# Kernel tuning notes

Measured on AMD Instinct MI355X. Metric: run time of the kernel, lower is better.

The kernel has to match this reference:

```python
import jax, jax.numpy as jnp
import numpy as np

D_MODEL = 1024
NUM_HEADS = 16
HEAD_DIM = D_MODEL // NUM_HEADS


def setup_inputs() -> dict:
    key = jax.random.key(0)
    ks = jax.random.split(key, 11)
    B, S, D = 2, 2048, D_MODEL
    scale = 1.0 / np.sqrt(D)
    inp = {
        "q": jax.random.normal(ks[0], (B, S, D), dtype=jnp.float32),
        "k": jax.random.normal(ks[1], (B, S, D), dtype=jnp.float32),
        "v": jax.random.normal(ks[2], (B, S, D), dtype=jnp.float32),
        # torch nn.Linear weights are [out, in]; y = x @ W.T + b
        "Wq": jax.random.normal(ks[3], (D, D), dtype=jnp.float32) * scale,
        "bq": jnp.zeros((D,), dtype=jnp.float32),
        "Wk": jax.random.normal(ks[4], (D, D), dtype=jnp.float32) * scale,
        "bk": jnp.zeros((D,), dtype=jnp.float32),
        "Wv": jax.random.normal(ks[5], (D, D), dtype=jnp.float32) * scale,
        "bv": jnp.zeros((D,), dtype=jnp.float32),
        "Wo": jax.random.normal(ks[6], (D, D), dtype=jnp.float32) * scale,
        "bo": jnp.zeros((D,), dtype=jnp.float32),
    }
    return inp


def _split_heads(x):
    B, S, D = x.shape
    return x.reshape(B, S, NUM_HEADS, HEAD_DIM).transpose(0, 2, 1, 3)  # [B,H,S,hd]


def reference(q, k, v, Wq, bq, Wk, bk, Wv, bv, Wo, bo):
    B, S, D = q.shape
    qh = _split_heads(q @ Wq.T + bq)
    kh = _split_heads(k @ Wk.T + bk)
    vh = _split_heads(v @ Wv.T + bv)
    # scores: [B,H,S,S], causal mask, softmax
    scores = jnp.einsum("bhqd,bhkd->bhqk", qh, kh) / jnp.sqrt(
        jnp.asarray(HEAD_DIM, dtype=qh.dtype))
    causal = jnp.tril(jnp.ones((S, S), dtype=bool))
    scores = jnp.where(causal[None, None], scores, -jnp.inf)
    attn = jax.nn.softmax(scores, axis=-1)
    out = jnp.einsum("bhqk,bhkd->bhqd", attn, vh)  # [B,H,S,hd]
    out = out.transpose(0, 2, 1, 3).reshape(B, S, D)
    return out @ Wo.T + bo
```

## Files before the change

kernel.cpp:

```cpp
#include <hip/hip_runtime.h>
#include <hip/hip_bf16.h>
#include <cstdint>
#include <cstddef>

typedef __bf16 bf16;
typedef __bf16 bf16x2 __attribute__((ext_vector_type(2)));
typedef __bf16 bf16x4 __attribute__((ext_vector_type(4)));
typedef __bf16 bf16x8 __attribute__((ext_vector_type(8)));
typedef float f32x4 __attribute__((ext_vector_type(4)));
typedef float f32x16 __attribute__((ext_vector_type(16)));
typedef unsigned int u32x4 __attribute__((ext_vector_type(4)));

#define S_LEN 2048
#define DM 1024
#define NH 16
#define HD 64
#define NQKV (4096 * 1024)
#define NW (1024 * 1024)
#define QK_SCALE 0.18033688011112042f

__device__ __forceinline__ void gload_lds16(const bf16* g, bf16* l) {
  __builtin_amdgcn_global_load_lds(
      (const __attribute__((address_space(1))) void*)g,
      (__attribute__((address_space(3))) void*)l, 16, 0, 0);
}

__device__ __forceinline__ unsigned packbf(float lo, float hi) {
  bf16x2 t;
  t[0] = (bf16)lo;
  t[1] = (bf16)hi;
  return __builtin_bit_cast(unsigned, t);
}

__device__ __forceinline__ void pl32swap(unsigned& a, unsigned& b) {
#if __has_builtin(__builtin_amdgcn_permlane32_swap)
  auto r = __builtin_amdgcn_permlane32_swap((int)a, (int)b, false, false);
  a = (unsigned)r[0];
  b = (unsigned)r[1];
#else
  asm volatile("v_permlane32_swap_b32 %0, %1" : "+v"(a), "+v"(b));
#endif
}

__global__ __launch_bounds__(256) void cvt_all(
    const float* __restrict__ q, const float* __restrict__ k, const float* __restrict__ v,
    const float* __restrict__ Wq, const float* __restrict__ Wk, const float* __restrict__ Wv,
    const float* __restrict__ Wo, bf16* __restrict__ out) {
  const size_t i = ((size_t)blockIdx.x * 256 + threadIdx.x) * 8;
  const float* src;
  size_t off;
  if (i < (size_t)NQKV) { src = q; off = i; }
  else if (i < 2ull * NQKV) { src = k; off = i - NQKV; }
  else if (i < 3ull * NQKV) { src = v; off = i - 2ull * NQKV; }
  else {
    const size_t j = i - 3ull * NQKV;
    if (j < (size_t)NW) { src = Wq; off = j; }
    else if (j < 2ull * NW) { src = Wk; off = j - NW; }
    else if (j < 3ull * NW) { src = Wv; off = j - 2ull * NW; }
    else { src = Wo; off = j - 3ull * NW; }
  }
  const float4 a = *(const float4*)(src + off);
  const float4 b = *(const float4*)(src + off + 4);
  bf16x8 o;
  o[0] = (bf16)a.x; o[1] = (bf16)a.y; o[2] = (bf16)a.z; o[3] = (bf16)a.w;
  o[4] = (bf16)b.x; o[5] = (bf16)b.y; o[6] = (bf16)b.z; o[7] = (bf16)b.w;
  *(bf16x8*)(out + i) = o;
}

template <int MODE>
__global__ __launch_bounds__(256, 2) void gemm_bt(
    const bf16* __restrict__ A, const bf16* __restrict__ W,
    const float* __restrict__ bias0, const float* __restrict__ bias1,
    const float* __restrict__ bias2, void* __restrict__ Out,
    int M, int N, int K, float scale) {
  __shared__ __align__(16) bf16 sm[2 * 128 * 64];
  bf16* Asl = sm;
  bf16* Bsl = sm + 128 * 64;
  const int tid = threadIdx.x;
  const int lane = tid & 63, w = tid >> 6;
  const int wr = w >> 1, wc = w & 1;
  const int r16 = lane & 15, grp = lane >> 4;

  int flat = blockIdx.y * gridDim.x + blockIdx.x;
  const int cpx = (gridDim.x * gridDim.y) >> 3;
  flat = (flat & 7) * cpx + (flat >> 3);
  const int m0 = (flat / gridDim.x) * 128;
  const int n0 = (flat % gridDim.x) * 128;

  const int seg = n0 >> 10;
  const bf16* Ab = (MODE == 3) ? A + (size_t)seg * NQKV : A;

  f32x4 acc[4][4] = {};

  const int nk = K >> 6;
  for (int t = 0; t < nk; ++t) {
    const int k0 = t << 6;
    __syncthreads();
#pragma unroll
    for (int j = 0; j < 4; ++j) {
      const int lin = j * 256 + tid;
      const int rr = lin >> 3;
      const int cc = (lin & 7) * 8;
      gload_lds16(&Ab[(size_t)(m0 + rr) * K + k0 + cc], &Asl[lin * 8]);
      gload_lds16(&W[(size_t)(n0 + rr) * K + k0 + cc], &Bsl[lin * 8]);
    }
    __syncthreads();
#pragma unroll
    for (int kk = 0; kk < 2; ++kk) {
      bf16x8 af[4], bfr[4];
#pragma unroll
      for (int m = 0; m < 4; ++m)
        af[m] = *(const bf16x8*)&Asl[(wr * 64 + m * 16 + r16) * 64 + kk * 32 + grp * 8];
#pragma unroll
      for (int n = 0; n < 4; ++n)
        bfr[n] = *(const bf16x8*)&Bsl[(wc * 64 + n * 16 + r16) * 64 + kk * 32 + grp * 8];
#pragma unroll
      for (int m = 0; m < 4; ++m)
#pragma unroll
        for (int n = 0; n < 4; ++n)
          acc[m][n] = __builtin_amdgcn_mfma_f32_16x16x32_bf16(af[m], bfr[n], acc[m][n], 0, 0, 0);
    }
  }

  const float* bp = (MODE == 3) ? (seg == 0 ? bias0 : (seg == 1 ? bias1 : bias2)) : bias0;
  const float sc = (MODE == 3) ? (seg == 0 ? scale : 1.0f) : scale;

  if (MODE == 3 && seg == 2) {
    __syncthreads();
    bf16* T = sm + w * (32 * 76);
    const int b = (m0 + wr * 64) >> 11;
    const int srow0 = (m0 + wr * 64) & 2047;
    bf16* base2 = (bf16*)Out + 2 * (size_t)NQKV;
#pragma unroll
    for (int p = 0; p < 2; ++p) {
#pragma unroll
      for (int nn = 0; nn < 2; ++nn) {
        const int n = 2 * p + nn;
#pragma unroll
        for (int mq = 0; mq < 4; ++mq)
#pragma unroll
          for (int r = 0; r < 4; ++r) {
            const int d_l = nn * 16 + r16;
            const int s_l = mq * 16 + grp * 4 + r;
            const int cs = (n0 + wc * 64 + n * 16 + r16) & 1023;
            T[d_l * 76 + s_l] = (bf16)(acc[mq][n][r] + bp[cs]);
          }
      }
      __syncthreads();
#pragma unroll
      for (int j = 0; j < 4; ++j) {
        const int d_l = j * 8 + (lane >> 3);
        const int scnk = lane & 7;
        const uint2 lo = *(const uint2*)&T[d_l * 76 + scnk * 8];
        const uint2 hi = *(const uint2*)&T[d_l * 76 + scnk * 8 + 4];
        const int cs = (n0 + wc * 64 + p * 32 + d_l) & 1023;
        const int hh = cs >> 6, dd = cs & 63;
        bf16* dst = base2 + ((size_t)(b * NH + hh) * HD + dd) * S_LEN + srow0 + scnk * 8;
        uint4 val; val.x = lo.x; val.y = lo.y; val.z = hi.x; val.w = hi.y;
        *(uint4*)dst = val;
      }
      __syncthreads();
    }
    return;
  }

#pragma unroll
  for (int m = 0; m < 4; ++m) {
#pragma unroll
    for (int n = 0; n < 4; ++n) {
#pragma unroll
      for (int r = 0; r < 4; ++r) {
        const int row = m0 + wr * 64 + m * 16 + grp * 4 + r;
        const int col = n0 + wc * 64 + n * 16 + r16;
        const int cs = col & 1023;
        const float v = (acc[m][n][r] + bp[cs]) * sc;
        if (MODE == 3) {
          const int b = row >> 11, s = row & 2047, h = cs >> 6, d = cs & 63;
          bf16* base = (bf16*)Out + (size_t)seg * NQKV;
          base[((size_t)(b * NH + h) * S_LEN + s) * HD + d] = (bf16)v;
        } else {
          ((float*)Out)[(size_t)row * N + col] = v;
        }
      }
    }
  }
}

__global__ __launch_bounds__(256, 2) void attn_fwd9(
    const bf16* __restrict__ Qh, const bf16* __restrict__ Kh,
    const bf16* __restrict__ Vt, bf16* __restrict__ AO) {
  __shared__ __align__(16) bf16 Kl[4][64 * 64];
  __shared__ __align__(16) bf16 Vl[4][64 * 64];

  const int tid = threadIdx.x;
  const int lane = tid & 63, w = tid >> 6;
  const int q31 = lane & 31, h = lane >> 5;
  const int qh = w >> 1, kh = w & 1;
  const int koff = kh << 5;

  const int bid = blockIdx.x;
  const int xcd = bid & 7;
  const int within = bid >> 3;
  const int bh = xcd * 4 + (within & 3);
  const int p = within >> 2;

  const bf16* Qb = Qh + (size_t)bh * S_LEN * HD;
  const bf16* Kb = Kh + (size_t)bh * S_LEN * HD;
  const bf16* Vb = Vt + (size_t)bh * HD * S_LEN;

  int stK[2], stV[2], stL[2];
#pragma unroll
  for (int i = 0; i < 2; ++i) {
    const int lin = i * 256 + tid;
    const int row = lin >> 3;
    const int colb = (lin & 7) * 16;
    const int scol = colb ^ ((row & 7) << 4);
    stK[i] = row * HD + (scol >> 1);
    stV[i] = row * S_LEN + (scol >> 1);
    stL[i] = lin * 8;
  }
  const int swz = (q31 & 7) << 4;

#define STAGE(t, buf)                                                          \
  {                                                                            \
    const bf16* kb_ = Kb + (size_t)(t) * 64 * HD;                              \
    const bf16* vb_ = Vb + (t) * 64;                                           \
    _Pragma("unroll") for (int i = 0; i < 2; ++i) {                            \
      gload_lds16(kb_ + stK[i], &Kl[buf][stL[i]]);                             \
      gload_lds16(vb_ + stV[i], &Vl[buf][stL[i]]);                             \
    }                                                                          \
  }

  auto run_chunk = [&](const int q0, const int nt) {
    const int q0w = q0 + (qh << 5);
    const int qg = q0w + q31;
    const int nt_w = (w == 1) ? nt - 1 : nt;
    const bool maskw = (w == 0) || (w == 3);

    bf16x8 qf[4];
#pragma unroll
    for (int ks = 0; ks < 4; ++ks)
      qf[ks] = *(const bf16x8*)&Qb[(size_t)qg * HD + ks * 16 + 8 * h];

    f32x16 acc0 = {}, acc1 = {};
    float m = -1e30f, l = 0.f;
    f32x16 pA = {}, pB = {};

    STAGE(0, 0)
    if (nt > 1) {
      STAGE(1, 1)
      asm volatile("s_waitcnt vmcnt(4)" ::: "memory");
    } else {
      asm volatile("s_waitcnt vmcnt(0)" ::: "memory");
    }
    __builtin_amdgcn_s_barrier();
    if (0 < nt_w) {
      bf16x8 kf[4];
#pragma unroll
      for (int ks = 0; ks < 4; ++ks) {
        const int c = (32 * ks + 16 * h) ^ swz;
        kf[ks] = *(const bf16x8*)((const char*)&Kl[0][0] + (koff + q31) * 128 + c);
      }
      __builtin_amdgcn_s_setprio(1);
#pragma unroll
      for (int ks = 0; ks < 4; ++ks)
        pA = __builtin_amdgcn_mfma_f32_32x32x16_bf16(kf[ks], qf[ks], pA, 0, 0, 0);
      __builtin_amdgcn_s_setprio(0);
    }

    auto body = [&](const int KT, f32x16& PC, f32x16& PN) {
      if (KT + 1 < nt) {
        if (KT + 2 < nt) {
          STAGE(KT + 2, (KT + 2) & 3)
          asm volatile("s_waitcnt vmcnt(4)" ::: "memory");
        } else {
          asm volatile("s_waitcnt vmcnt(0)" ::: "memory");
        }
        __builtin_amdgcn_s_barrier();
        if (KT + 1 < nt_w) {
          const char* KlN = (const char*)&Kl[(KT + 1) & 3][0];
          bf16x8 kf[4];
#pragma unroll
          for (int ks = 0; ks < 4; ++ks) {
            const int c = (32 * ks + 16 * h) ^ swz;
            kf[ks] = *(const bf16x8*)(KlN + (koff + q31) * 128 + c);
          }
          PN = {};
          __builtin_amdgcn_s_setprio(1);
#pragma unroll
          for (int ks = 0; ks < 4; ++ks)
            PN = __builtin_amdgcn_mfma_f32_32x32x16_bf16(kf[ks], qf[ks], PN, 0, 0, 0);
          __builtin_amdgcn_s_setprio(0);
        }
      }

      if (KT < nt_w) {
        const char* VlC = (const char*)&Vl[KT & 3][0];
        bf16x8 vf[4];
#pragma unroll
        for (int ks = 0; ks < 2; ++ks)
#pragma unroll
          for (int db = 0; db < 2; ++db) {
            const int c = (64 * kh + 32 * ks + 16 * h) ^ swz;
            vf[ks * 2 + db] = *(const bf16x8*)(VlC + (db * 32 + q31) * 128 + c);
          }

        if (maskw && KT == nt - 1) {
#pragma unroll
          for (int r = 0; r < 16; ++r) {
            const int key = (KT << 6) + koff + (r & 3) + 8 * (r >> 2) + 4 * h;
            if (key > qg) PC[r] = -1e30f;
          }
        }
        float t_[16];
#pragma unroll
        for (int r = 0; r < 16; ++r) t_[r] = PC[r];
#pragma unroll
        for (int s = 8; s >= 1; s >>= 1)
#pragma unroll
          for (int r = 0; r < s; ++r) t_[r] = fmaxf(t_[r], t_[r + s]);
        const float pmax = fmaxf(t_[0], __shfl_xor(t_[0], 32));
        if (!__all(pmax - m <= 8.0f)) {
          const float mn = fmaxf(m, pmax);
          const float al = exp2f(m - mn);
          m = mn;
          l *= al;
#pragma unroll
          for (int r = 0; r < 16; ++r) { acc0[r] *= al; acc1[r] *= al; }
        }
        float sv[16];
#pragma unroll
        for (int r = 0; r < 16; ++r) {
          PC[r] = exp2f(PC[r] - m);
          sv[r] = PC[r];
        }
#pragma unroll
        for (int s = 8; s >= 1; s >>= 1)
#pragma unroll
          for (int r = 0; r < s; ++r) sv[r] += sv[r + s];
        l += sv[0] + __shfl_xor(sv[0], 32);

        unsigned wv[8];
#pragma unroll
        for (int mm = 0; mm < 8; ++mm)
          wv[mm] = packbf(PC[2 * mm], PC[2 * mm + 1]);
        pl32swap(wv[0], wv[2]);
        pl32swap(wv[1], wv[3]);
        pl32swap(wv[4], wv[6]);
        pl32swap(wv[5], wv[7]);

        __builtin_amdgcn_s_setprio(1);
        {
          u32x4 pu0 = {wv[0], wv[1], wv[2], wv[3]};
          const bf16x8 pf0 = __builtin_bit_cast(bf16x8, pu0);
          acc0 = __builtin_amdgcn_mfma_f32_32x32x16_bf16(vf[0], pf0, acc0, 0, 0, 0);
          acc1 = __builtin_amdgcn_mfma_f32_32x32x16_bf16(vf[1], pf0, acc1, 0, 0, 0);
          u32x4 pu1 = {wv[4], wv[5], wv[6], wv[7]};
          const bf16x8 pf1 = __builtin_bit_cast(bf16x8, pu1);
          acc0 = __builtin_amdgcn_mfma_f32_32x32x16_bf16(vf[2], pf1, acc0, 0, 0, 0);
          acc1 = __builtin_amdgcn_mfma_f32_32x32x16_bf16(vf[3], pf1, acc1, 0, 0, 0);
        }
        __builtin_amdgcn_s_setprio(0);
      }
    };

    int kt = 0;
    for (; kt + 2 <= nt; kt += 2) {
      body(kt, pA, pB);
      body(kt + 1, pB, pA);
    }
    if (kt < nt) body(kt, pA, pB);

    float* scr = (float*)&Kl[0][0];
    float* s = scr + (size_t)qh * (64 * 33) + lane * 33;
    __syncthreads();
    if (kh) {
#pragma unroll
      for (int r = 0; r < 16; ++r) { s[r] = acc0[r]; s[16 + r] = acc1[r]; }
      s[32] = m;
    }
    float* sl = scr + 2 * (64 * 33) + (size_t)qh * 64 + lane;
    if (kh) *sl = l;
    __syncthreads();
    if (!kh) {
      const float m1 = s[32], l1 = *sl;
      const float mn = fmaxf(m, m1);
      const float a0 = exp2f(m - mn), a1 = exp2f(m1 - mn);
      const float linv = 1.0f / (a0 * l + a1 * l1);
      const int b = bh >> 4, hh = bh & 15;
      bf16* orow = AO + ((size_t)(b * S_LEN + qg)) * DM + hh * HD;
#pragma unroll
      for (int mm = 0; mm < 4; ++mm) {
        bf16x4 ov0, ov1;
#pragma unroll
        for (int t2 = 0; t2 < 4; ++t2) {
          ov0[t2] = (bf16)((a0 * acc0[4 * mm + t2] + a1 * s[4 * mm + t2]) * linv);
          ov1[t2] = (bf16)((a0 * acc1[4 * mm + t2] + a1 * s[16 + 4 * mm + t2]) * linv);
        }
        *(bf16x4*)&orow[8 * mm + 4 * h] = ov0;
        *(bf16x4*)&orow[32 + 8 * mm + 4 * h] = ov1;
      }
    }
    __syncthreads();
  };

  run_chunk(p << 6, p + 1);
  run_chunk((31 - p) << 6, 32 - p);
#undef STAGE
}

extern "C" void kernel_launch(void* const* d_in, const int* in_sizes, int n_in,
                              void* d_out, int out_size, void* d_ws, size_t ws_size,
                              hipStream_t stream) {
  const float* q  = (const float*)d_in[0];
  const float* k  = (const float*)d_in[1];
  const float* v  = (const float*)d_in[2];
  const float* Wq = (const float*)d_in[3];
  const float* bq = (const float*)d_in[4];
  const float* Wk = (const float*)d_in[5];
  const float* bk = (const float*)d_in[6];
  const float* Wv = (const float*)d_in[7];
  const float* bv = (const float*)d_in[8];
  const float* Wo = (const float*)d_in[9];
  const float* bo = (const float*)d_in[10];

  const int NTOK = 2 * S_LEN;

  bf16* qb  = (bf16*)d_ws;
  bf16* Wqb = qb + 3 * (size_t)NQKV;
  bf16* Wob = Wqb + 3 * (size_t)NW;
  bf16* Qh  = Wqb + 4 * (size_t)NW;
  bf16* Kh  = Qh + (size_t)NQKV;
  bf16* Vt  = Kh + (size_t)NQKV;
  bf16* AO  = Vt + (size_t)NQKV;

  const int cvt_blocks = (3 * NQKV + 4 * NW) / 8 / 256;
  cvt_all<<<cvt_blocks, 256, 0, stream>>>(q, k, v, Wq, Wk, Wv, Wo, qb);

  gemm_bt<3><<<dim3(3 * DM / 128, NTOK / 128), 256, 0, stream>>>(
      qb, Wqb, bq, bk, bv, Qh, NTOK, 3 * DM, DM, QK_SCALE);

  attn_fwd9<<<dim3(512), 256, 0, stream>>>(Qh, Kh, Vt, AO);

  gemm_bt<2><<<dim3(DM / 128, NTOK / 128), 256, 0, stream>>>(
      AO, Wob, bo, bo, bo, d_out, NTOK, DM, DM, 1.0f);
}
```

Baseline: 123.9 us.

## Process two key tiles per iteration with one barrier and joint softmax

Replaces the software-pipelined attention loop, which computed the next tile's QK^T while doing softmax on the current one, with a loop that handles two 64-key tiles per iteration. Each pair gets one barrier, two tiles of prefetch, a combined row max and one online-softmax rescale. This halves barriers and rescale checks. It gives up the QK/softmax overlap and waits for all loads (vmcnt(0)) before each pair, so load latency may be less hidden. The scratch layout for merging the two key halves is also changed to keep m and l per lane.

```diff
diff --git a/kernel.cpp b/kernel.cpp
--- a/kernel.cpp
+++ b/kernel.cpp
@@ -186,7 +186,7 @@
   }
 }
 
-__global__ __launch_bounds__(256, 2) void attn_fwd9(
+__global__ __launch_bounds__(256, 2) void attn_fwd11(
     const bf16* __restrict__ Qh, const bf16* __restrict__ Kh,
     const bf16* __restrict__ Vt, bf16* __restrict__ AO) {
   __shared__ __align__(16) bf16 Kl[4][64 * 64];
@@ -244,77 +244,78 @@
 
     f32x16 acc0 = {}, acc1 = {};
     float m = -1e30f, l = 0.f;
-    f32x16 pA = {}, pB = {};
 
     STAGE(0, 0)
-    if (nt > 1) {
-      STAGE(1, 1)
-      asm volatile("s_waitcnt vmcnt(4)" ::: "memory");
-    } else {
+    if (nt > 1) STAGE(1, 1)
+
+    const int npair = (nt + 1) >> 1;
+    for (int it = 0; it < npair; ++it) {
+      const int t0 = it << 1;
       asm volatile("s_waitcnt vmcnt(0)" ::: "memory");
-    }
-    __builtin_amdgcn_s_barrier();
-    if (0 < nt_w) {
-      bf16x8 kf[4];
-#pragma unroll
-      for (int ks = 0; ks < 4; ++ks) {
-        const int c = (32 * ks + 16 * h) ^ swz;
-        kf[ks] = *(const bf16x8*)((const char*)&Kl[0][0] + (koff + q31) * 128 + c);
-      }
-      __builtin_amdgcn_s_setprio(1);
-#pragma unroll
-      for (int ks = 0; ks < 4; ++ks)
-        pA = __builtin_amdgcn_mfma_f32_32x32x16_bf16(kf[ks], qf[ks], pA, 0, 0, 0);
-      __builtin_amdgcn_s_setprio(0);
-    }
-
-    auto body = [&](const int KT, f32x16& PC, f32x16& PN) {
-      if (KT + 1 < nt) {
-        if (KT + 2 < nt) {
-          STAGE(KT + 2, (KT + 2) & 3)
-          asm volatile("s_waitcnt vmcnt(4)" ::: "memory");
-        } else {
-          asm volatile("s_waitcnt vmcnt(0)" ::: "memory");
-        }
-        __builtin_amdgcn_s_barrier();
-        if (KT + 1 < nt_w) {
-          const char* KlN = (const char*)&Kl[(KT + 1) & 3][0];
+      __builtin_amdgcn_s_barrier();
+      if (t0 + 2 < nt) STAGE(t0 + 2, (t0 + 2) & 3)
+      if (t0 + 3 < nt) STAGE(t0 + 3, (t0 + 3) & 3)
+
+      const bool live1 = (t0 + 1 < nt_w);
+      if (t0 < nt_w) {
+        const char* Kl0 = (const char*)&Kl[t0 & 3][0];
+        const char* Vl0 = (const char*)&Vl[t0 & 3][0];
+        const char* Kl1 = (const char*)&Kl[(t0 + 1) & 3][0];
+        const char* Vl1 = (const char*)&Vl[(t0 + 1) & 3][0];
+
+        f32x16 s0 = {}, s1 = {};
+        {
           bf16x8 kf[4];
 #pragma unroll
           for (int ks = 0; ks < 4; ++ks) {
             const int c = (32 * ks + 16 * h) ^ swz;
-            kf[ks] = *(const bf16x8*)(KlN + (koff + q31) * 128 + c);
-          }
-          PN = {};
+            kf[ks] = *(const bf16x8*)(Kl0 + (koff + q31) * 128 + c);
+          }
           __builtin_amdgcn_s_setprio(1);
 #pragma unroll
           for (int ks = 0; ks < 4; ++ks)
-            PN = __builtin_amdgcn_mfma_f32_32x32x16_bf16(kf[ks], qf[ks], PN, 0, 0, 0);
+            s0 = __builtin_amdgcn_mfma_f32_32x32x16_bf16(kf[ks], qf[ks], s0, 0, 0, 0);
           __builtin_amdgcn_s_setprio(0);
         }
-      }
-
-      if (KT < nt_w) {
-        const char* VlC = (const char*)&Vl[KT & 3][0];
-        bf16x8 vf[4];
-#pragma unroll
-        for (int ks = 0; ks < 2; ++ks)
-#pragma unroll
-          for (int db = 0; db < 2; ++db) {
-            const int c = (64 * kh + 32 * ks + 16 * h) ^ swz;
-            vf[ks * 2 + db] = *(const bf16x8*)(VlC + (db * 32 + q31) * 128 + c);
-          }
-
-        if (maskw && KT == nt - 1) {
-#pragma unroll
-          for (int r = 0; r < 16; ++r) {
-            const int key = (KT << 6) + koff + (r & 3) + 8 * (r >> 2) + 4 * h;
-            if (key > qg) PC[r] = -1e30f;
-          }
-        }
+        if (live1) {
+          bf16x8 kf[4];
+#pragma unroll
+          for (int ks = 0; ks < 4; ++ks) {
+            const int c = (32 * ks + 16 * h) ^ swz;
+            kf[ks] = *(const bf16x8*)(Kl1 + (koff + q31) * 128 + c);
+          }
+          __builtin_amdgcn_s_setprio(1);
+#pragma unroll
+          for (int ks = 0; ks < 4; ++ks)
+            s1 = __builtin_amdgcn_mfma_f32_32x32x16_bf16(kf[ks], qf[ks], s1, 0, 0, 0);
+          __builtin_amdgcn_s_setprio(0);
+        }
+
+        if (maskw) {
+          if (t0 == nt - 1) {
+#pragma unroll
+            for (int r = 0; r < 16; ++r) {
+              const int key = (t0 << 6) + koff + (r & 3) + 8 * (r >> 2) + 4 * h;
+              if (key > qg) s0[r] = -1e30f;
+            }
+          }
+          if (live1 && t0 + 1 == nt - 1) {
+#pragma unroll
+            for (int r = 0; r < 16; ++r) {
+              const int key = ((t0 + 1) << 6) + koff + (r & 3) + 8 * (r >> 2) + 4 * h;
+              if (key > qg) s1[r] = -1e30f;
+            }
+          }
+        }
+
         float t_[16];
-#pragma unroll
-        for (int r = 0; r < 16; ++r) t_[r] = PC[r];
+        if (live1) {
+#pragma unroll
+          for (int r = 0; r < 16; ++r) t_[r] = fmaxf(s0[r], s1[r]);
+        } else {
+#pragma unroll
+          for (int r = 0; r < 16; ++r) t_[r] = s0[r];
+        }
 #pragma unroll
         for (int s = 8; s >= 1; s >>= 1)
 #pragma unroll
@@ -331,8 +332,15 @@
         float sv[16];
 #pragma unroll
         for (int r = 0; r < 16; ++r) {
-          PC[r] = exp2f(PC[r] - m);
-          sv[r] = PC[r];
+          s0[r] = exp2f(s0[r] - m);
+          sv[r] = s0[r];
+        }
+        if (live1) {
+#pragma unroll
+          for (int r = 0; r < 16; ++r) {
+            s1[r] = exp2f(s1[r] - m);
+            sv[r] += s1[r];
+          }
         }
 #pragma unroll
         for (int s = 8; s >= 1; s >>= 1)
@@ -340,17 +348,24 @@
           for (int r = 0; r < s; ++r) sv[r] += sv[r + s];
         l += sv[0] + __shfl_xor(sv[0], 32);
 
-        unsigned wv[8];
-#pragma unroll
-        for (int mm = 0; mm < 8; ++mm)
-          wv[mm] = packbf(PC[2 * mm], PC[2 * mm + 1]);
-        pl32swap(wv[0], wv[2]);
-        pl32swap(wv[1], wv[3]);
-        pl32swap(wv[4], wv[6]);
-        pl32swap(wv[5], wv[7]);
-
-        __builtin_amdgcn_s_setprio(1);
         {
+          unsigned wv[8];
+#pragma unroll
+          for (int mm = 0; mm < 8; ++mm)
+            wv[mm] = packbf(s0[2 * mm], s0[2 * mm + 1]);
+          pl32swap(wv[0], wv[2]);
+          pl32swap(wv[1], wv[3]);
+          pl32swap(wv[4], wv[6]);
+          pl32swap(wv[5], wv[7]);
+          bf16x8 vf[4];
+#pragma unroll
+          for (int ks = 0; ks < 2; ++ks)
+#pragma unroll
+            for (int db = 0; db < 2; ++db) {
+              const int c = (64 * kh + 32 * ks + 16 * h) ^ swz;
+              vf[ks * 2 + db] = *(const bf16x8*)(Vl0 + (db * 32 + q31) * 128 + c);
+            }
+          __builtin_amdgcn_s_setprio(1);
           u32x4 pu0 = {wv[0], wv[1], wv[2], wv[3]};
           const bf16x8 pf0 = __builtin_bit_cast(bf16x8, pu0);
           acc0 = __builtin_amdgcn_mfma_f32_32x32x16_bf16(vf[0], pf0, acc0, 0, 0, 0);
@@ -359,31 +374,51 @@
           const bf16x8 pf1 = __builtin_bit_cast(bf16x8, pu1);
           acc0 = __builtin_amdgcn_mfma_f32_32x32x16_bf16(vf[2], pf1, acc0, 0, 0, 0);
           acc1 = __builtin_amdgcn_mfma_f32_32x32x16_bf16(vf[3], pf1, acc1, 0, 0, 0);
-        }
-        __builtin_amdgcn_s_setprio(0);
+          __builtin_amdgcn_s_setprio(0);
+        }
+        if (live1) {
+          unsigned wv[8];
+#pragma unroll
+          for (int mm = 0; mm < 8; ++mm)
+            wv[mm] = packbf(s1[2 * mm], s1[2 * mm + 1]);
+          pl32swap(wv[0], wv[2]);
+          pl32swap(wv[1], wv[3]);
+          pl32swap(wv[4], wv[6]);
+          pl32swap(wv[5], wv[7]);
+          bf16x8 vf[4];
+#pragma unroll
+          for (int ks = 0; ks < 2; ++ks)
+#pragma unroll
+            for (int db = 0; db < 2; ++db) {
+              const int c = (64 * kh + 32 * ks + 16 * h) ^ swz;
+              vf[ks * 2 + db] = *(const bf16x8*)(Vl1 + (db * 32 + q31) * 128 + c);
+            }
+          __builtin_amdgcn_s_setprio(1);
+          u32x4 pu0 = {wv[0], wv[1], wv[2], wv[3]};
+          const bf16x8 pf0 = __builtin_bit_cast(bf16x8, pu0);
+          acc0 = __builtin_amdgcn_mfma_f32_32x32x16_bf16(vf[0], pf0, acc0, 0, 0, 0);
+          acc1 = __builtin_amdgcn_mfma_f32_32x32x16_bf16(vf[1], pf0, acc1, 0, 0, 0);
+          u32x4 pu1 = {wv[4], wv[5], wv[6], wv[7]};
+          const bf16x8 pf1 = __builtin_bit_cast(bf16x8, pu1);
+          acc0 = __builtin_amdgcn_mfma_f32_32x32x16_bf16(vf[2], pf1, acc0, 0, 0, 0);
+          acc1 = __builtin_amdgcn_mfma_f32_32x32x16_bf16(vf[3], pf1, acc1, 0, 0, 0);
+          __builtin_amdgcn_s_setprio(0);
+        }
       }
-    };
-
-    int kt = 0;
-    for (; kt + 2 <= nt; kt += 2) {
-      body(kt, pA, pB);
-      body(kt + 1, pB, pA);
-    }
-    if (kt < nt) body(kt, pA, pB);
+    }
 
     float* scr = (float*)&Kl[0][0];
-    float* s = scr + (size_t)qh * (64 * 33) + lane * 33;
+    float* s = scr + (size_t)qh * (64 * 34) + lane * 34;
     __syncthreads();
     if (kh) {
 #pragma unroll
       for (int r = 0; r < 16; ++r) { s[r] = acc0[r]; s[16 + r] = acc1[r]; }
       s[32] = m;
-    }
-    float* sl = scr + 2 * (64 * 33) + (size_t)qh * 64 + lane;
-    if (kh) *sl = l;
+      s[33] = l;
+    }
     __syncthreads();
     if (!kh) {
-      const float m1 = s[32], l1 = *sl;
+      const float m1 = s[32], l1 = s[33];
       const float mn = fmaxf(m, m1);
       const float a0 = exp2f(m - mn), a1 = exp2f(m1 - mn);
       const float linv = 1.0f / (a0 * l + a1 * l1);
@@ -440,7 +475,7 @@
   gemm_bt<3><<<dim3(3 * DM / 128, NTOK / 128), 256, 0, stream>>>(
       qb, Wqb, bq, bk, bv, Qh, NTOK, 3 * DM, DM, QK_SCALE);
 
-  attn_fwd9<<<dim3(512), 256, 0, stream>>>(Qh, Kh, Vt, AO);
+  attn_fwd11<<<dim3(512), 256, 0, stream>>>(Qh, Kh, Vt, AO);
 
   gemm_bt<2><<<dim3(DM / 128, NTOK / 128), 256, 0, stream>>>(
       AO, Wob, bo, bo, bo, d_out, NTOK, DM, DM, 1.0f);
```

Result: no change. 123.9 us (+0.1%).
